# Kernel tuning notes

Hardware: AMD Instinct MI355X
Metric: run time of the kernel (lower is better)

The kernel has to match this reference:

```python
import jax, jax.numpy as jnp
import numpy as np


def setup_inputs() -> dict:
    key = jax.random.key(0)
    k1, k2 = jax.random.split(key)
    x = jax.random.normal(k1, (32, 256, 32, 32), dtype=jnp.float32)
    emb = jax.random.uniform(k2, (256, 2048), dtype=jnp.float32)
    return {"x": x, "emb": emb}


def reference(x, emb):
    # x: (B, D, H, W), emb: (D, K)
    B, D = x.shape[0], x.shape[1]
    spatial = x.shape[2:]
    K = emb.shape[1]
    # flatten latents: (N, D) with N = B*H*W
    xf = jnp.moveaxis(x, 1, -1).reshape(-1, D)
    d2 = (jnp.sum(xf * xf, axis=-1, keepdims=True)
          - 2.0 * (xf @ emb)
          + jnp.sum(emb * emb, axis=0))  # (N, K)
    argmin = jnp.argmin(d2, axis=-1)  # (N,)
    q = jnp.take(emb.T, argmin, axis=0)  # (N, D) nearest codes
    out = q.reshape(B, *spatial, D)
    out = jnp.moveaxis(out, -1, 1)  # (B, D, H, W)
    return out
```

## Files before the change

### kernel.cpp

```cpp
#include <hip/hip_runtime.h>


typedef __attribute__((ext_vector_type(8))) _Float16 half8v;
typedef __attribute__((ext_vector_type(16))) float floatx16;
typedef unsigned int uint;
typedef unsigned short ushort;

#define DD 256
#define KK 2048
#define SS 1024
#define NN 32768
#define MT 128
#define NTT 256
#define CD 32
#define LDA 40
#define MFMA_F16 __builtin_amdgcn_mfma_f32_32x32x16_f16

union HU { _Float16 f; ushort u; };

__device__ __forceinline__ void split16(float v, ushort& h, ushort& l) {
    HU a, b;
    a.f = (_Float16)v;
    b.f = (_Float16)(v - (float)a.f);
    h = a.u; l = b.u;
}

__device__ __forceinline__ uint pk(ushort a, ushort b) {
    return (uint)a | ((uint)b << 16);
}

__global__ __launch_bounds__(256) void hn_kernel(const float* __restrict__ emb,
                                                 float* __restrict__ hn) {
    __shared__ float red[256];
    const int tid = threadIdx.x;
    const int k = blockIdx.x * 32 + (tid & 31);
    const int j = tid >> 5;
    float a = 0.f;
#pragma unroll
    for (int i = 0; i < 32; ++i) {
        float e = emb[(size_t)(j * 32 + i) * KK + k];
        a += e * e;
    }
    red[tid] = a;
    __syncthreads();
    if (j == 0) {
        float s = a;
#pragma unroll
        for (int g = 1; g < 8; ++g) s += red[g * 32 + (tid & 31)];
        hn[k] = 0.5f * s;
    }
}

__global__ __launch_bounds__(256) void pack_emb(const float* __restrict__ emb,
                                                uint4* __restrict__ epk) {
    int idx = blockIdx.x * 256 + threadIdx.x;
    int k = idx & (KK - 1);
    int q = idx >> 11;
    ushort h[8], l[8];
#pragma unroll
    for (int j = 0; j < 8; ++j) {
        float e = emb[(size_t)(8 * q + j) * KK + k];
        split16(e, h[j], l[j]);
    }
    uint4 H, L;
    H.x = pk(h[0], h[1]); H.y = pk(h[2], h[3]);
    H.z = pk(h[4], h[5]); H.w = pk(h[6], h[7]);
    L.x = pk(l[0], l[1]); L.y = pk(l[2], l[3]);
    L.z = pk(l[4], l[5]); L.w = pk(l[6], l[7]);
    epk[(size_t)(q * 2 + 0) * KK + k] = H;
    epk[(size_t)(q * 2 + 1) * KK + k] = L;
}

template <bool PRE>
__global__ __launch_bounds__(1024, 4) void vq_fused(
        const float* __restrict__ x, const float* __restrict__ emb,
        const float* __restrict__ hn, const uint4* __restrict__ epk,
        float* __restrict__ out) {
    __shared__ ushort Ah[2][MT * LDA], Al[2][MT * LDA];
    __shared__ ushort Bh[2][NTT * LDA], Bl[2][NTT * LDA];
    __shared__ float sv[4][MT];
    __shared__ int   sc[4][MT];
    __shared__ int   bc[MT];

    const int tid = threadIdx.x;
    const int lane = tid & 63;
    const int wid = tid >> 6;
    const int colk = lane & 31;
    const int half = lane >> 5;
    const int wm = (wid & 3) * 32;
    const int wn = (wid >> 2) * 64;

    const int base_n = blockIdx.x * MT;
    const int bq = base_n >> 10;
    const int sb = base_n & (SS - 1);

    const int lat_a = tid & 127;
    const int d2a = tid >> 7;
    const int cod_b = tid & 255;
    const int pB = (tid >> 8) & 1;
    const int oB = tid >> 9;

    const float* xA = x + ((size_t)bq * DD + 2 * d2a) * SS + sb + lat_a;

    floatx16 acc[2];
#pragma unroll
    for (int j = 0; j < 2; ++j) acc[j] = (floatx16)(0.0f);

    float bestv[16];
    int bestc[16];
#pragma unroll
    for (int r = 0; r < 16; ++r) { bestv[r] = 3.4e38f; bestc[r] = 0; }

    float fa[4];
    uint4 ub0, ub1;
    float fb[16];

    fa[0] = xA[0];
    fa[1] = xA[SS];
    fa[2] = xA[(size_t)16 * SS];
    fa[3] = xA[(size_t)17 * SS];
    if constexpr (PRE) {
        const int qg = 2 * oB;
        ub0 = epk[(size_t)(qg * 2 + pB) * KK + cod_b];
        ub1 = epk[(size_t)((qg + 1) * 2 + pB) * KK + cod_b];
    } else {
#pragma unroll
        for (int i = 0; i < 16; ++i)
            fb[i] = emb[(size_t)(oB * 16 + i) * KK + cod_b];
    }
    {
        ushort h0, l0, h1, l1, h2, l2, h3, l3;
        split16(fa[0], h0, l0); split16(fa[1], h1, l1);
        split16(fa[2], h2, l2); split16(fa[3], h3, l3);
        *reinterpret_cast<uint*>(&Ah[0][lat_a * LDA + 2 * d2a]) = pk(h0, h1);
        *reinterpret_cast<uint*>(&Al[0][lat_a * LDA + 2 * d2a]) = pk(l0, l1);
        *reinterpret_cast<uint*>(&Ah[0][lat_a * LDA + 2 * d2a + 16]) = pk(h2, h3);
        *reinterpret_cast<uint*>(&Al[0][lat_a * LDA + 2 * d2a + 16]) = pk(l2, l3);
        uint4 w0, w1;
        if constexpr (PRE) {
            w0 = ub0; w1 = ub1;
        } else {
            ushort h[16], l[16];
#pragma unroll
            for (int i = 0; i < 16; ++i) split16(fb[i], h[i], l[i]);
            const ushort* s = pB ? l : h;
            w0.x = pk(s[0], s[1]);  w0.y = pk(s[2], s[3]);
            w0.z = pk(s[4], s[5]);  w0.w = pk(s[6], s[7]);
            w1.x = pk(s[8], s[9]);  w1.y = pk(s[10], s[11]);
            w1.z = pk(s[12], s[13]); w1.w = pk(s[14], s[15]);
        }
        ushort* Bp = pB ? &Bl[0][0] : &Bh[0][0];
        *reinterpret_cast<uint4*>(&Bp[cod_b * LDA + oB * 16]) = w0;
        *reinterpret_cast<uint4*>(&Bp[cod_b * LDA + oB * 16 + 8]) = w1;
    }
    __syncthreads();

    for (int c = 0; c < 64; ++c) {
        const int cur = c & 1, nxt = cur ^ 1;
        if (c < 63) {
            const int c1 = c + 1;
            const int kt1 = c1 >> 3;
            const int dt1 = (c1 & 7) * CD;
            fa[0] = xA[(size_t)(dt1 + 0) * SS];
            fa[1] = xA[(size_t)(dt1 + 1) * SS];
            fa[2] = xA[(size_t)(dt1 + 16) * SS];
            fa[3] = xA[(size_t)(dt1 + 17) * SS];
            if constexpr (PRE) {
                const int qg = (dt1 >> 3) + 2 * oB;
                const size_t kb = (size_t)kt1 * NTT + cod_b;
                ub0 = epk[(size_t)(qg * 2 + pB) * KK + kb];
                ub1 = epk[(size_t)((qg + 1) * 2 + pB) * KK + kb];
            } else {
#pragma unroll
                for (int i = 0; i < 16; ++i)
                    fb[i] = emb[(size_t)(dt1 + oB * 16 + i) * KK
                                + kt1 * NTT + cod_b];
            }
        }
        const int fo = colk * LDA + half * 8;
        {
            half8v ah = *reinterpret_cast<const half8v*>(&Ah[cur][fo + wm * LDA]);
            half8v al = *reinterpret_cast<const half8v*>(&Al[cur][fo + wm * LDA]);
            half8v bh0 = *reinterpret_cast<const half8v*>(&Bh[cur][fo + wn * LDA]);
            half8v bh1 = *reinterpret_cast<const half8v*>(&Bh[cur][fo + (wn + 32) * LDA]);
            half8v bl0 = *reinterpret_cast<const half8v*>(&Bl[cur][fo + wn * LDA]);
            half8v bl1 = *reinterpret_cast<const half8v*>(&Bl[cur][fo + (wn + 32) * LDA]);
            acc[0] = MFMA_F16(ah, bh0, acc[0], 0, 0, 0);
            acc[0] = MFMA_F16(ah, bl0, acc[0], 0, 0, 0);
            acc[0] = MFMA_F16(al, bh0, acc[0], 0, 0, 0);
            acc[1] = MFMA_F16(ah, bh1, acc[1], 0, 0, 0);
            acc[1] = MFMA_F16(ah, bl1, acc[1], 0, 0, 0);
            acc[1] = MFMA_F16(al, bh1, acc[1], 0, 0, 0);
        }
        {
            half8v ah = *reinterpret_cast<const half8v*>(&Ah[cur][fo + wm * LDA + 16]);
            half8v al = *reinterpret_cast<const half8v*>(&Al[cur][fo + wm * LDA + 16]);
            half8v bh0 = *reinterpret_cast<const half8v*>(&Bh[cur][fo + wn * LDA + 16]);
            half8v bh1 = *reinterpret_cast<const half8v*>(&Bh[cur][fo + (wn + 32) * LDA + 16]);
            half8v bl0 = *reinterpret_cast<const half8v*>(&Bl[cur][fo + wn * LDA + 16]);
            half8v bl1 = *reinterpret_cast<const half8v*>(&Bl[cur][fo + (wn + 32) * LDA + 16]);
            acc[0] = MFMA_F16(ah, bh0, acc[0], 0, 0, 0);
            acc[0] = MFMA_F16(ah, bl0, acc[0], 0, 0, 0);
            acc[0] = MFMA_F16(al, bh0, acc[0], 0, 0, 0);
            acc[1] = MFMA_F16(ah, bh1, acc[1], 0, 0, 0);
            acc[1] = MFMA_F16(ah, bl1, acc[1], 0, 0, 0);
            acc[1] = MFMA_F16(al, bh1, acc[1], 0, 0, 0);
        }

        if (c < 63) {
            ushort h0, l0, h1, l1, h2, l2, h3, l3;
            split16(fa[0], h0, l0); split16(fa[1], h1, l1);
            split16(fa[2], h2, l2); split16(fa[3], h3, l3);
            *reinterpret_cast<uint*>(&Ah[nxt][lat_a * LDA + 2 * d2a]) = pk(h0, h1);
            *reinterpret_cast<uint*>(&Al[nxt][lat_a * LDA + 2 * d2a]) = pk(l0, l1);
            *reinterpret_cast<uint*>(&Ah[nxt][lat_a * LDA + 2 * d2a + 16]) = pk(h2, h3);
            *reinterpret_cast<uint*>(&Al[nxt][lat_a * LDA + 2 * d2a + 16]) = pk(l2, l3);
            uint4 w0, w1;
            if constexpr (PRE) {
                w0 = ub0; w1 = ub1;
            } else {
                ushort h[16], l[16];
#pragma unroll
                for (int i = 0; i < 16; ++i) split16(fb[i], h[i], l[i]);
                const ushort* s = pB ? l : h;
                w0.x = pk(s[0], s[1]);  w0.y = pk(s[2], s[3]);
                w0.z = pk(s[4], s[5]);  w0.w = pk(s[6], s[7]);
                w1.x = pk(s[8], s[9]);  w1.y = pk(s[10], s[11]);
                w1.z = pk(s[12], s[13]); w1.w = pk(s[14], s[15]);
            }
            ushort* Bp = pB ? &Bl[nxt][0] : &Bh[nxt][0];
            *reinterpret_cast<uint4*>(&Bp[cod_b * LDA + oB * 16]) = w0;
            *reinterpret_cast<uint4*>(&Bp[cod_b * LDA + oB * 16 + 8]) = w1;
        }
        if ((c & 7) == 7) {
            const int kt = c >> 3;
            const int cd0 = kt * NTT + wn + colk;
            const int cd1 = cd0 + 32;
            const float h0 = hn[cd0];
            const float h1 = hn[cd1];
#pragma unroll
            for (int r = 0; r < 16; ++r) {
                float s0 = h0 - acc[0][r];
                float s1 = h1 - acc[1][r];
                float v = s0; int cd = cd0;
                if (s1 < s0) { v = s1; cd = cd1; }
                if (v < bestv[r]) { bestv[r] = v; bestc[r] = cd; }
                acc[0][r] = 0.f;
                acc[1][r] = 0.f;
            }
        }
        __syncthreads();
    }

#pragma unroll
    for (int r = 0; r < 16; ++r) {
        float v = bestv[r];
        int cd = bestc[r];
#pragma unroll
        for (int mk = 1; mk < 32; mk <<= 1) {
            float ov = __shfl_xor(v, mk);
            int oc = __shfl_xor(cd, mk);
            if (ov < v || (ov == v && oc < cd)) { v = ov; cd = oc; }
        }
        if (colk == 0) {
            const int row = (r & 3) + 8 * (r >> 2) + 4 * half;
            sv[wid >> 2][wm + row] = v;
            sc[wid >> 2][wm + row] = cd;
        }
    }
    __syncthreads();
    if (tid < MT) {
        float v = sv[0][tid]; int cd = sc[0][tid];
#pragma unroll
        for (int g = 1; g < 4; ++g) {
            float ov = sv[g][tid]; int oc = sc[g][tid];
            if (ov < v || (ov == v && oc < cd)) { v = ov; cd = oc; }
        }
        bc[tid] = cd;
    }
    __syncthreads();
    {
        const int mq = tid & 31;
        const int dg = tid >> 5;
        const int k0 = bc[mq * 4 + 0];
        const int k1 = bc[mq * 4 + 1];
        const int k2 = bc[mq * 4 + 2];
        const int k3 = bc[mq * 4 + 3];
#pragma unroll 4
        for (int dd = 0; dd < 8; ++dd) {
            const int d = dg * 8 + dd;
            const float* er = emb + (size_t)d * KK;
            float4 o = make_float4(er[k0], er[k1], er[k2], er[k3]);
            reinterpret_cast<float4*>(&out[((size_t)bq * DD + d) * SS + sb])[mq] = o;
        }
    }
}

extern "C" void kernel_launch(void* const* d_in, const int* in_sizes, int n_in,
                              void* d_out, int out_size, void* d_ws, size_t ws_size,
                              hipStream_t stream) {
    const float* x = (const float*)d_in[0];
    const float* emb = (const float*)d_in[1];
    float* out = (float*)d_out;
    float* hn = (float*)d_ws;
    uint4* epk = (uint4*)((char*)d_ws + KK * sizeof(float));

    const size_t need = (size_t)KK * 4 + (size_t)32 * 2 * KK * 16;

    hipLaunchKernelGGL(hn_kernel, dim3(KK / 32), dim3(256), 0, stream, emb, hn);
    if (ws_size >= need) {
        hipLaunchKernelGGL(pack_emb, dim3(65536 / 256), dim3(256), 0, stream,
                           emb, epk);
        hipLaunchKernelGGL((vq_fused<true>), dim3(NN / MT), dim3(1024), 0, stream,
                           x, emb, hn, epk, out);
    } else {
        hipLaunchKernelGGL((vq_fused<false>), dim3(NN / MT), dim3(1024), 0, stream,
                           x, emb, hn, epk, out);
    }
}
```

Measured before the change: 216.1 us.

## Use 512-thread blocks with 64x64 warp tiles and XOR-swizzled LDS layout

```diff
diff --git a/kernel.cpp b/kernel.cpp
--- a/kernel.cpp
+++ b/kernel.cpp
@@ -13,7 +13,7 @@
 #define MT 128
 #define NTT 256
 #define CD 32
-#define LDA 40
+#define LDB 32
 #define MFMA_F16 __builtin_amdgcn_mfma_f32_32x32x16_f16
 
 union HU { _Float16 f; ushort u; };
@@ -27,6 +27,10 @@
 
 __device__ __forceinline__ uint pk(ushort a, ushort b) {
     return (uint)a | ((uint)b << 16);
+}
+
+__device__ __forceinline__ int swz(int row, int slot) {
+    return row * LDB + ((slot ^ ((row >> 1) & 3)) << 3);
 }
 
 __global__ __launch_bounds__(256) void hn_kernel(const float* __restrict__ emb,
@@ -72,12 +76,12 @@
 }
 
 template <bool PRE>
-__global__ __launch_bounds__(1024, 4) void vq_fused(
+__global__ __launch_bounds__(512, 2) void vq_fused(
         const float* __restrict__ x, const float* __restrict__ emb,
         const float* __restrict__ hn, const uint4* __restrict__ epk,
         float* __restrict__ out) {
-    __shared__ ushort Ah[2][MT * LDA], Al[2][MT * LDA];
-    __shared__ ushort Bh[2][NTT * LDA], Bl[2][NTT * LDA];
+    __shared__ ushort Ah[2][MT * LDB], Al[2][MT * LDB];
+    __shared__ ushort Bh[2][NTT * LDB], Bl[2][NTT * LDB];
     __shared__ float sv[4][MT];
     __shared__ int   sc[4][MT];
     __shared__ int   bc[MT];
@@ -87,71 +91,83 @@
     const int wid = tid >> 6;
     const int colk = lane & 31;
     const int half = lane >> 5;
-    const int wm = (wid & 3) * 32;
-    const int wn = (wid >> 2) * 64;
+    const int wm = (wid & 1) * 64;
+    const int wn = (wid >> 1) * 64;
 
     const int base_n = blockIdx.x * MT;
     const int bq = base_n >> 10;
     const int sb = base_n & (SS - 1);
 
     const int lat_a = tid & 127;
-    const int d2a = tid >> 7;
+    const int qa = tid >> 7;
     const int cod_b = tid & 255;
-    const int pB = (tid >> 8) & 1;
-    const int oB = tid >> 9;
-
-    const float* xA = x + ((size_t)bq * DD + 2 * d2a) * SS + sb + lat_a;
-
-    floatx16 acc[2];
-#pragma unroll
-    for (int j = 0; j < 2; ++j) acc[j] = (floatx16)(0.0f);
-
-    float bestv[16];
-    int bestc[16];
-#pragma unroll
-    for (int r = 0; r < 16; ++r) { bestv[r] = 3.4e38f; bestc[r] = 0; }
-
-    float fa[4];
-    uint4 ub0, ub1;
+    const int pB = tid >> 8;
+    const int oB = tid >> 8;
+
+    const float* xA = x + (size_t)bq * DD * SS + sb + lat_a;
+
+    floatx16 acc[2][2];
+#pragma unroll
+    for (int i = 0; i < 2; ++i)
+#pragma unroll
+        for (int j = 0; j < 2; ++j) acc[i][j] = (floatx16)(0.0f);
+
+    float bestv[2][16];
+    int bestc[2][16];
+#pragma unroll
+    for (int t = 0; t < 2; ++t)
+#pragma unroll
+        for (int r = 0; r < 16; ++r) { bestv[t][r] = 3.4e38f; bestc[t][r] = 0; }
+
+    float fa[8];
+    uint4 uq[4];
     float fb[16];
 
-    fa[0] = xA[0];
-    fa[1] = xA[SS];
-    fa[2] = xA[(size_t)16 * SS];
-    fa[3] = xA[(size_t)17 * SS];
+#pragma unroll
+    for (int j = 0; j < 8; ++j) fa[j] = xA[(size_t)(8 * qa + j) * SS];
     if constexpr (PRE) {
-        const int qg = 2 * oB;
-        ub0 = epk[(size_t)(qg * 2 + pB) * KK + cod_b];
-        ub1 = epk[(size_t)((qg + 1) * 2 + pB) * KK + cod_b];
+#pragma unroll
+        for (int s = 0; s < 4; ++s)
+            uq[s] = epk[(size_t)(s * 2 + pB) * KK + cod_b];
     } else {
 #pragma unroll
         for (int i = 0; i < 16; ++i)
             fb[i] = emb[(size_t)(oB * 16 + i) * KK + cod_b];
     }
     {
-        ushort h0, l0, h1, l1, h2, l2, h3, l3;
-        split16(fa[0], h0, l0); split16(fa[1], h1, l1);
-        split16(fa[2], h2, l2); split16(fa[3], h3, l3);
-        *reinterpret_cast<uint*>(&Ah[0][lat_a * LDA + 2 * d2a]) = pk(h0, h1);
-        *reinterpret_cast<uint*>(&Al[0][lat_a * LDA + 2 * d2a]) = pk(l0, l1);
-        *reinterpret_cast<uint*>(&Ah[0][lat_a * LDA + 2 * d2a + 16]) = pk(h2, h3);
-        *reinterpret_cast<uint*>(&Al[0][lat_a * LDA + 2 * d2a + 16]) = pk(l2, l3);
-        uint4 w0, w1;
+        ushort h[8], l[8];
+#pragma unroll
+        for (int j = 0; j < 8; ++j) split16(fa[j], h[j], l[j]);
+        uint4 H, L;
+        H.x = pk(h[0], h[1]); H.y = pk(h[2], h[3]);
+        H.z = pk(h[4], h[5]); H.w = pk(h[6], h[7]);
+        L.x = pk(l[0], l[1]); L.y = pk(l[2], l[3]);
+        L.z = pk(l[4], l[5]); L.w = pk(l[6], l[7]);
+        *reinterpret_cast<uint4*>(&Ah[0][swz(lat_a, qa)]) = H;
+        *reinterpret_cast<uint4*>(&Al[0][swz(lat_a, qa)]) = L;
         if constexpr (PRE) {
-            w0 = ub0; w1 = ub1;
+            ushort* Bp = pB ? &Bl[0][0] : &Bh[0][0];
+#pragma unroll
+            for (int s = 0; s < 4; ++s)
+                *reinterpret_cast<uint4*>(&Bp[swz(cod_b, s)]) = uq[s];
         } else {
-            ushort h[16], l[16];
-#pragma unroll
-            for (int i = 0; i < 16; ++i) split16(fb[i], h[i], l[i]);
-            const ushort* s = pB ? l : h;
-            w0.x = pk(s[0], s[1]);  w0.y = pk(s[2], s[3]);
-            w0.z = pk(s[4], s[5]);  w0.w = pk(s[6], s[7]);
-            w1.x = pk(s[8], s[9]);  w1.y = pk(s[10], s[11]);
-            w1.z = pk(s[12], s[13]); w1.w = pk(s[14], s[15]);
-        }
-        ushort* Bp = pB ? &Bl[0][0] : &Bh[0][0];
-        *reinterpret_cast<uint4*>(&Bp[cod_b * LDA + oB * 16]) = w0;
-        *reinterpret_cast<uint4*>(&Bp[cod_b * LDA + oB * 16 + 8]) = w1;
+            ushort hh[16], ll[16];
+#pragma unroll
+            for (int i = 0; i < 16; ++i) split16(fb[i], hh[i], ll[i]);
+            uint4 w;
+            w.x = pk(hh[0], hh[1]);  w.y = pk(hh[2], hh[3]);
+            w.z = pk(hh[4], hh[5]);  w.w = pk(hh[6], hh[7]);
+            *reinterpret_cast<uint4*>(&Bh[0][swz(cod_b, oB * 2)]) = w;
+            w.x = pk(hh[8], hh[9]);  w.y = pk(hh[10], hh[11]);
+            w.z = pk(hh[12], hh[13]); w.w = pk(hh[14], hh[15]);
+            *reinterpret_cast<uint4*>(&Bh[0][swz(cod_b, oB * 2 + 1)]) = w;
+            w.x = pk(ll[0], ll[1]);  w.y = pk(ll[2], ll[3]);
+            w.z = pk(ll[4], ll[5]);  w.w = pk(ll[6], ll[7]);
+            *reinterpret_cast<uint4*>(&Bl[0][swz(cod_b, oB * 2)]) = w;
+            w.x = pk(ll[8], ll[9]);  w.y = pk(ll[10], ll[11]);
+            w.z = pk(ll[12], ll[13]); w.w = pk(ll[14], ll[15]);
+            *reinterpret_cast<uint4*>(&Bl[0][swz(cod_b, oB * 2 + 1)]) = w;
+        }
     }
     __syncthreads();
 
@@ -161,15 +177,15 @@
             const int c1 = c + 1;
             const int kt1 = c1 >> 3;
             const int dt1 = (c1 & 7) * CD;
-            fa[0] = xA[(size_t)(dt1 + 0) * SS];
-            fa[1] = xA[(size_t)(dt1 + 1) * SS];
-            fa[2] = xA[(size_t)(dt1 + 16) * SS];
-            fa[3] = xA[(size_t)(dt1 + 17) * SS];
+#pragma unroll
+            for (int j = 0; j < 8; ++j)
+                fa[j] = xA[(size_t)(dt1 + 8 * qa + j) * SS];
             if constexpr (PRE) {
-                const int qg = (dt1 >> 3) + 2 * oB;
+                const int qg = dt1 >> 3;
                 const size_t kb = (size_t)kt1 * NTT + cod_b;
-                ub0 = epk[(size_t)(qg * 2 + pB) * KK + kb];
-                ub1 = epk[(size_t)((qg + 1) * 2 + pB) * KK + kb];
+#pragma unroll
+                for (int s = 0; s < 4; ++s)
+                    uq[s] = epk[(size_t)((qg + s) * 2 + pB) * KK + kb];
             } else {
 #pragma unroll
                 for (int i = 0; i < 16; ++i)
@@ -177,60 +193,69 @@
                                 + kt1 * NTT + cod_b];
             }
         }
-        const int fo = colk * LDA + half * 8;
-        {
-            half8v ah = *reinterpret_cast<const half8v*>(&Ah[cur][fo + wm * LDA]);
-            half8v al = *reinterpret_cast<const half8v*>(&Al[cur][fo + wm * LDA]);
-            half8v bh0 = *reinterpret_cast<const half8v*>(&Bh[cur][fo + wn * LDA]);
-            half8v bh1 = *reinterpret_cast<const half8v*>(&Bh[cur][fo + (wn + 32) * LDA]);
-            half8v bl0 = *reinterpret_cast<const half8v*>(&Bl[cur][fo + wn * LDA]);
-            half8v bl1 = *reinterpret_cast<const half8v*>(&Bl[cur][fo + (wn + 32) * LDA]);
-            acc[0] = MFMA_F16(ah, bh0, acc[0], 0, 0, 0);
-            acc[0] = MFMA_F16(ah, bl0, acc[0], 0, 0, 0);
-            acc[0] = MFMA_F16(al, bh0, acc[0], 0, 0, 0);
-            acc[1] = MFMA_F16(ah, bh1, acc[1], 0, 0, 0);
-            acc[1] = MFMA_F16(ah, bl1, acc[1], 0, 0, 0);
-            acc[1] = MFMA_F16(al, bh1, acc[1], 0, 0, 0);
-        }
-        {
-            half8v ah = *reinterpret_cast<const half8v*>(&Ah[cur][fo + wm * LDA + 16]);
-            half8v al = *reinterpret_cast<const half8v*>(&Al[cur][fo + wm * LDA + 16]);
-            half8v bh0 = *reinterpret_cast<const half8v*>(&Bh[cur][fo + wn * LDA + 16]);
-            half8v bh1 = *reinterpret_cast<const half8v*>(&Bh[cur][fo + (wn + 32) * LDA + 16]);
-            half8v bl0 = *reinterpret_cast<const half8v*>(&Bl[cur][fo + wn * LDA + 16]);
-            half8v bl1 = *reinterpret_cast<const half8v*>(&Bl[cur][fo + (wn + 32) * LDA + 16]);
-            acc[0] = MFMA_F16(ah, bh0, acc[0], 0, 0, 0);
-            acc[0] = MFMA_F16(ah, bl0, acc[0], 0, 0, 0);
-            acc[0] = MFMA_F16(al, bh0, acc[0], 0, 0, 0);
-            acc[1] = MFMA_F16(ah, bh1, acc[1], 0, 0, 0);
-            acc[1] = MFMA_F16(ah, bl1, acc[1], 0, 0, 0);
-            acc[1] = MFMA_F16(al, bh1, acc[1], 0, 0, 0);
+#pragma unroll
+        for (int t = 0; t < 2; ++t) {
+            const int sA = t * 2 + half;
+            half8v ah0 = *reinterpret_cast<const half8v*>(&Ah[cur][swz(wm + colk, sA)]);
+            half8v ah1 = *reinterpret_cast<const half8v*>(&Ah[cur][swz(wm + 32 + colk, sA)]);
+            half8v al0 = *reinterpret_cast<const half8v*>(&Al[cur][swz(wm + colk, sA)]);
+            half8v al1 = *reinterpret_cast<const half8v*>(&Al[cur][swz(wm + 32 + colk, sA)]);
+            half8v bh0 = *reinterpret_cast<const half8v*>(&Bh[cur][swz(wn + colk, sA)]);
+            half8v bh1 = *reinterpret_cast<const half8v*>(&Bh[cur][swz(wn + 32 + colk, sA)]);
+            half8v bl0 = *reinterpret_cast<const half8v*>(&Bl[cur][swz(wn + colk, sA)]);
+            half8v bl1 = *reinterpret_cast<const half8v*>(&Bl[cur][swz(wn + 32 + colk, sA)]);
+
+            acc[0][0] = MFMA_F16(ah0, bh0, acc[0][0], 0, 0, 0);
+            acc[0][0] = MFMA_F16(ah0, bl0, acc[0][0], 0, 0, 0);
+            acc[0][0] = MFMA_F16(al0, bh0, acc[0][0], 0, 0, 0);
+
+            acc[0][1] = MFMA_F16(ah0, bh1, acc[0][1], 0, 0, 0);
+            acc[0][1] = MFMA_F16(ah0, bl1, acc[0][1], 0, 0, 0);
+            acc[0][1] = MFMA_F16(al0, bh1, acc[0][1], 0, 0, 0);
+
+            acc[1][0] = MFMA_F16(ah1, bh0, acc[1][0], 0, 0, 0);
+            acc[1][0] = MFMA_F16(ah1, bl0, acc[1][0], 0, 0, 0);
+            acc[1][0] = MFMA_F16(al1, bh0, acc[1][0], 0, 0, 0);
+
+            acc[1][1] = MFMA_F16(ah1, bh1, acc[1][1], 0, 0, 0);
+            acc[1][1] = MFMA_F16(ah1, bl1, acc[1][1], 0, 0, 0);
+            acc[1][1] = MFMA_F16(al1, bh1, acc[1][1], 0, 0, 0);
         }
 
         if (c < 63) {
-            ushort h0, l0, h1, l1, h2, l2, h3, l3;
-            split16(fa[0], h0, l0); split16(fa[1], h1, l1);
-            split16(fa[2], h2, l2); split16(fa[3], h3, l3);
-            *reinterpret_cast<uint*>(&Ah[nxt][lat_a * LDA + 2 * d2a]) = pk(h0, h1);
-            *reinterpret_cast<uint*>(&Al[nxt][lat_a * LDA + 2 * d2a]) = pk(l0, l1);
-            *reinterpret_cast<uint*>(&Ah[nxt][lat_a * LDA + 2 * d2a + 16]) = pk(h2, h3);
-            *reinterpret_cast<uint*>(&Al[nxt][lat_a * LDA + 2 * d2a + 16]) = pk(l2, l3);
-            uint4 w0, w1;
+            ushort h[8], l[8];
+#pragma unroll
+            for (int j = 0; j < 8; ++j) split16(fa[j], h[j], l[j]);
+            uint4 H, L;
+            H.x = pk(h[0], h[1]); H.y = pk(h[2], h[3]);
+            H.z = pk(h[4], h[5]); H.w = pk(h[6], h[7]);
+            L.x = pk(l[0], l[1]); L.y = pk(l[2], l[3]);
+            L.z = pk(l[4], l[5]); L.w = pk(l[6], l[7]);
+            *reinterpret_cast<uint4*>(&Ah[nxt][swz(lat_a, qa)]) = H;
+            *reinterpret_cast<uint4*>(&Al[nxt][swz(lat_a, qa)]) = L;
             if constexpr (PRE) {
-                w0 = ub0; w1 = ub1;
+                ushort* Bp = pB ? &Bl[nxt][0] : &Bh[nxt][0];
+#pragma unroll
+                for (int s = 0; s < 4; ++s)
+                    *reinterpret_cast<uint4*>(&Bp[swz(cod_b, s)]) = uq[s];
             } else {
-                ushort h[16], l[16];
-#pragma unroll
-                for (int i = 0; i < 16; ++i) split16(fb[i], h[i], l[i]);
-                const ushort* s = pB ? l : h;
-                w0.x = pk(s[0], s[1]);  w0.y = pk(s[2], s[3]);
-                w0.z = pk(s[4], s[5]);  w0.w = pk(s[6], s[7]);
-                w1.x = pk(s[8], s[9]);  w1.y = pk(s[10], s[11]);
-                w1.z = pk(s[12], s[13]); w1.w = pk(s[14], s[15]);
-            }
-            ushort* Bp = pB ? &Bl[nxt][0] : &Bh[nxt][0];
-            *reinterpret_cast<uint4*>(&Bp[cod_b * LDA + oB * 16]) = w0;
-            *reinterpret_cast<uint4*>(&Bp[cod_b * LDA + oB * 16 + 8]) = w1;
+                ushort hh[16], ll[16];
+#pragma unroll
+                for (int i = 0; i < 16; ++i) split16(fb[i], hh[i], ll[i]);
+                uint4 w;
+                w.x = pk(hh[0], hh[1]);  w.y = pk(hh[2], hh[3]);
+                w.z = pk(hh[4], hh[5]);  w.w = pk(hh[6], hh[7]);
+                *reinterpret_cast<uint4*>(&Bh[nxt][swz(cod_b, oB * 2)]) = w;
+                w.x = pk(hh[8], hh[9]);  w.y = pk(hh[10], hh[11]);
+                w.z = pk(hh[12], hh[13]); w.w = pk(hh[14], hh[15]);
+                *reinterpret_cast<uint4*>(&Bh[nxt][swz(cod_b, oB * 2 + 1)]) = w;
+                w.x = pk(ll[0], ll[1]);  w.y = pk(ll[2], ll[3]);
+                w.z = pk(ll[4], ll[5]);  w.w = pk(ll[6], ll[7]);
+                *reinterpret_cast<uint4*>(&Bl[nxt][swz(cod_b, oB * 2)]) = w;
+                w.x = pk(ll[8], ll[9]);  w.y = pk(ll[10], ll[11]);
+                w.z = pk(ll[12], ll[13]); w.w = pk(ll[14], ll[15]);
+                *reinterpret_cast<uint4*>(&Bl[nxt][swz(cod_b, oB * 2 + 1)]) = w;
+            }
         }
         if ((c & 7) == 7) {
             const int kt = c >> 3;
@@ -239,33 +264,39 @@
             const float h0 = hn[cd0];
             const float h1 = hn[cd1];
 #pragma unroll
-            for (int r = 0; r < 16; ++r) {
-                float s0 = h0 - acc[0][r];
-                float s1 = h1 - acc[1][r];
-                float v = s0; int cd = cd0;
-                if (s1 < s0) { v = s1; cd = cd1; }
-                if (v < bestv[r]) { bestv[r] = v; bestc[r] = cd; }
-                acc[0][r] = 0.f;
-                acc[1][r] = 0.f;
+            for (int tm = 0; tm < 2; ++tm) {
+#pragma unroll
+                for (int r = 0; r < 16; ++r) {
+                    float s0 = h0 - acc[tm][0][r];
+                    float s1 = h1 - acc[tm][1][r];
+                    float v = s0; int cd = cd0;
+                    if (s1 < s0) { v = s1; cd = cd1; }
+                    if (v < bestv[tm][r]) { bestv[tm][r] = v; bestc[tm][r] = cd; }
+                    acc[tm][0][r] = 0.f;
+                    acc[tm][1][r] = 0.f;
+                }
             }
         }
         __syncthreads();
     }
 
 #pragma unroll
-    for (int r = 0; r < 16; ++r) {
-        float v = bestv[r];
-        int cd = bestc[r];
-#pragma unroll
-        for (int mk = 1; mk < 32; mk <<= 1) {
-            float ov = __shfl_xor(v, mk);
-            int oc = __shfl_xor(cd, mk);
-            if (ov < v || (ov == v && oc < cd)) { v = ov; cd = oc; }
-        }
-        if (colk == 0) {
-            const int row = (r & 3) + 8 * (r >> 2) + 4 * half;
-            sv[wid >> 2][wm + row] = v;
-            sc[wid >> 2][wm + row] = cd;
+    for (int tm = 0; tm < 2; ++tm) {
+#pragma unroll
+        for (int r = 0; r < 16; ++r) {
+            float v = bestv[tm][r];
+            int cd = bestc[tm][r];
+#pragma unroll
+            for (int mk = 1; mk < 32; mk <<= 1) {
+                float ov = __shfl_xor(v, mk);
+                int oc = __shfl_xor(cd, mk);
+                if (ov < v || (ov == v && oc < cd)) { v = ov; cd = oc; }
+            }
+            if (colk == 0) {
+                const int row = (r & 3) + 8 * (r >> 2) + 4 * half;
+                sv[wid >> 1][wm + tm * 32 + row] = v;
+                sc[wid >> 1][wm + tm * 32 + row] = cd;
+            }
         }
     }
     __syncthreads();
@@ -287,8 +318,8 @@
         const int k2 = bc[mq * 4 + 2];
         const int k3 = bc[mq * 4 + 3];
 #pragma unroll 4
-        for (int dd = 0; dd < 8; ++dd) {
-            const int d = dg * 8 + dd;
+        for (int dd = 0; dd < 16; ++dd) {
+            const int d = dg * 16 + dd;
             const float* er = emb + (size_t)d * KK;
             float4 o = make_float4(er[k0], er[k1], er[k2], er[k3]);
             reinterpret_cast<float4*>(&out[((size_t)bq * DD + d) * SS + sb])[mq] = o;
@@ -311,10 +342,10 @@
     if (ws_size >= need) {
         hipLaunchKernelGGL(pack_emb, dim3(65536 / 256), dim3(256), 0, stream,
                            emb, epk);
-        hipLaunchKernelGGL((vq_fused<true>), dim3(NN / MT), dim3(1024), 0, stream,
+        hipLaunchKernelGGL((vq_fused<true>), dim3(NN / MT), dim3(512), 0, stream,
                            x, emb, hn, epk, out);
     } else {
-        hipLaunchKernelGGL((vq_fused<false>), dim3(NN / MT), dim3(1024), 0, stream,
+        hipLaunchKernelGGL((vq_fused<false>), dim3(NN / MT), dim3(512), 0, stream,
                            x, emb, hn, epk, out);
     }
 }
```

After: 220.3 us. About the same (+2.0%).

## Prefetch global tiles two stages ahead with register double-buffering

Applied to the files above, without the earlier changes.

```diff
diff --git a/kernel.cpp b/kernel.cpp
--- a/kernel.cpp
+++ b/kernel.cpp
@@ -111,144 +111,113 @@
 #pragma unroll
     for (int r = 0; r < 16; ++r) { bestv[r] = 3.4e38f; bestc[r] = 0; }
 
-    float fa[4];
-    uint4 ub0, ub1;
-    float fb[16];
-
-    fa[0] = xA[0];
-    fa[1] = xA[SS];
-    fa[2] = xA[(size_t)16 * SS];
-    fa[3] = xA[(size_t)17 * SS];
-    if constexpr (PRE) {
-        const int qg = 2 * oB;
-        ub0 = epk[(size_t)(qg * 2 + pB) * KK + cod_b];
-        ub1 = epk[(size_t)((qg + 1) * 2 + pB) * KK + cod_b];
-    } else {
-#pragma unroll
-        for (int i = 0; i < 16; ++i)
-            fb[i] = emb[(size_t)(oB * 16 + i) * KK + cod_b];
-    }
-    {
+    float fa0[4], fa1[4];
+    uint4 u00, u01, u10, u11;
+    float fb0[16], fb1[16];
+
+    auto issueA = [&](int c, float (&fa)[4]) {
+        const int dt = (c & 7) * CD;
+        fa[0] = xA[(size_t)(dt + 0) * SS];
+        fa[1] = xA[(size_t)(dt + 1) * SS];
+        fa[2] = xA[(size_t)(dt + 16) * SS];
+        fa[3] = xA[(size_t)(dt + 17) * SS];
+    };
+    auto issueB = [&](int c, uint4& a0, uint4& a1, float (&fb)[16]) {
+        const int kt = c >> 3;
+        const int dt = (c & 7) * CD;
+        if constexpr (PRE) {
+            const int qg = (dt >> 3) + 2 * oB;
+            const size_t kb = (size_t)kt * NTT + cod_b;
+            a0 = epk[(size_t)(qg * 2 + pB) * KK + kb];
+            a1 = epk[(size_t)((qg + 1) * 2 + pB) * KK + kb];
+        } else {
+#pragma unroll
+            for (int i = 0; i < 16; ++i)
+                fb[i] = emb[(size_t)(dt + oB * 16 + i) * KK
+                            + (size_t)kt * NTT + cod_b];
+        }
+    };
+    auto stageWrite = [&](int nxt, float (&fa)[4], uint4& a0, uint4& a1,
+                          float (&fb)[16]) {
         ushort h0, l0, h1, l1, h2, l2, h3, l3;
         split16(fa[0], h0, l0); split16(fa[1], h1, l1);
         split16(fa[2], h2, l2); split16(fa[3], h3, l3);
-        *reinterpret_cast<uint*>(&Ah[0][lat_a * LDA + 2 * d2a]) = pk(h0, h1);
-        *reinterpret_cast<uint*>(&Al[0][lat_a * LDA + 2 * d2a]) = pk(l0, l1);
-        *reinterpret_cast<uint*>(&Ah[0][lat_a * LDA + 2 * d2a + 16]) = pk(h2, h3);
-        *reinterpret_cast<uint*>(&Al[0][lat_a * LDA + 2 * d2a + 16]) = pk(l2, l3);
+        *reinterpret_cast<uint*>(&Ah[nxt][lat_a * LDA + 2 * d2a]) = pk(h0, h1);
+        *reinterpret_cast<uint*>(&Al[nxt][lat_a * LDA + 2 * d2a]) = pk(l0, l1);
+        *reinterpret_cast<uint*>(&Ah[nxt][lat_a * LDA + 2 * d2a + 16]) = pk(h2, h3);
+        *reinterpret_cast<uint*>(&Al[nxt][lat_a * LDA + 2 * d2a + 16]) = pk(l2, l3);
         uint4 w0, w1;
         if constexpr (PRE) {
-            w0 = ub0; w1 = ub1;
+            w0 = a0; w1 = a1;
         } else {
-            ushort h[16], l[16];
-#pragma unroll
-            for (int i = 0; i < 16; ++i) split16(fb[i], h[i], l[i]);
-            const ushort* s = pB ? l : h;
-            w0.x = pk(s[0], s[1]);  w0.y = pk(s[2], s[3]);
-            w0.z = pk(s[4], s[5]);  w0.w = pk(s[6], s[7]);
-            w1.x = pk(s[8], s[9]);  w1.y = pk(s[10], s[11]);
+            ushort hh[16], ll[16];
+#pragma unroll
+            for (int i = 0; i < 16; ++i) split16(fb[i], hh[i], ll[i]);
+            const ushort* s = pB ? ll : hh;
+            w0.x = pk(s[0], s[1]);   w0.y = pk(s[2], s[3]);
+            w0.z = pk(s[4], s[5]);   w0.w = pk(s[6], s[7]);
+            w1.x = pk(s[8], s[9]);   w1.y = pk(s[10], s[11]);
             w1.z = pk(s[12], s[13]); w1.w = pk(s[14], s[15]);
         }
-        ushort* Bp = pB ? &Bl[0][0] : &Bh[0][0];
+        ushort* Bp = pB ? &Bl[nxt][0] : &Bh[nxt][0];
         *reinterpret_cast<uint4*>(&Bp[cod_b * LDA + oB * 16]) = w0;
         *reinterpret_cast<uint4*>(&Bp[cod_b * LDA + oB * 16 + 8]) = w1;
-    }
-    __syncthreads();
-
-    for (int c = 0; c < 64; ++c) {
-        const int cur = c & 1, nxt = cur ^ 1;
-        if (c < 63) {
-            const int c1 = c + 1;
-            const int kt1 = c1 >> 3;
-            const int dt1 = (c1 & 7) * CD;
-            fa[0] = xA[(size_t)(dt1 + 0) * SS];
-            fa[1] = xA[(size_t)(dt1 + 1) * SS];
-            fa[2] = xA[(size_t)(dt1 + 16) * SS];
-            fa[3] = xA[(size_t)(dt1 + 17) * SS];
-            if constexpr (PRE) {
-                const int qg = (dt1 >> 3) + 2 * oB;
-                const size_t kb = (size_t)kt1 * NTT + cod_b;
-                ub0 = epk[(size_t)(qg * 2 + pB) * KK + kb];
-                ub1 = epk[(size_t)((qg + 1) * 2 + pB) * KK + kb];
-            } else {
-#pragma unroll
-                for (int i = 0; i < 16; ++i)
-                    fb[i] = emb[(size_t)(dt1 + oB * 16 + i) * KK
-                                + kt1 * NTT + cod_b];
-            }
-        }
+    };
+    auto compute = [&](int cur) {
         const int fo = colk * LDA + half * 8;
-        {
-            half8v ah = *reinterpret_cast<const half8v*>(&Ah[cur][fo + wm * LDA]);
-            half8v al = *reinterpret_cast<const half8v*>(&Al[cur][fo + wm * LDA]);
-            half8v bh0 = *reinterpret_cast<const half8v*>(&Bh[cur][fo + wn * LDA]);
-            half8v bh1 = *reinterpret_cast<const half8v*>(&Bh[cur][fo + (wn + 32) * LDA]);
-            half8v bl0 = *reinterpret_cast<const half8v*>(&Bl[cur][fo + wn * LDA]);
-            half8v bl1 = *reinterpret_cast<const half8v*>(&Bl[cur][fo + (wn + 32) * LDA]);
+#pragma unroll
+        for (int t = 0; t < 2; ++t) {
+            const int o = t * 16;
+            half8v ah = *reinterpret_cast<const half8v*>(&Ah[cur][fo + wm * LDA + o]);
+            half8v al = *reinterpret_cast<const half8v*>(&Al[cur][fo + wm * LDA + o]);
+            half8v bh0 = *reinterpret_cast<const half8v*>(&Bh[cur][fo + wn * LDA + o]);
+            half8v bh1 = *reinterpret_cast<const half8v*>(&Bh[cur][fo + (wn + 32) * LDA + o]);
+            half8v bl0 = *reinterpret_cast<const half8v*>(&Bl[cur][fo + wn * LDA + o]);
+            half8v bl1 = *reinterpret_cast<const half8v*>(&Bl[cur][fo + (wn + 32) * LDA + o]);
+
             acc[0] = MFMA_F16(ah, bh0, acc[0], 0, 0, 0);
             acc[0] = MFMA_F16(ah, bl0, acc[0], 0, 0, 0);
             acc[0] = MFMA_F16(al, bh0, acc[0], 0, 0, 0);
+
             acc[1] = MFMA_F16(ah, bh1, acc[1], 0, 0, 0);
             acc[1] = MFMA_F16(ah, bl1, acc[1], 0, 0, 0);
             acc[1] = MFMA_F16(al, bh1, acc[1], 0, 0, 0);
         }
-        {
-            half8v ah = *reinterpret_cast<const half8v*>(&Ah[cur][fo + wm * LDA + 16]);
-            half8v al = *reinterpret_cast<const half8v*>(&Al[cur][fo + wm * LDA + 16]);
-            half8v bh0 = *reinterpret_cast<const half8v*>(&Bh[cur][fo + wn * LDA + 16]);
-            half8v bh1 = *reinterpret_cast<const half8v*>(&Bh[cur][fo + (wn + 32) * LDA + 16]);
-            half8v bl0 = *reinterpret_cast<const half8v*>(&Bl[cur][fo + wn * LDA + 16]);
-            half8v bl1 = *reinterpret_cast<const half8v*>(&Bl[cur][fo + (wn + 32) * LDA + 16]);
-            acc[0] = MFMA_F16(ah, bh0, acc[0], 0, 0, 0);
-            acc[0] = MFMA_F16(ah, bl0, acc[0], 0, 0, 0);
-            acc[0] = MFMA_F16(al, bh0, acc[0], 0, 0, 0);
-            acc[1] = MFMA_F16(ah, bh1, acc[1], 0, 0, 0);
-            acc[1] = MFMA_F16(ah, bl1, acc[1], 0, 0, 0);
-            acc[1] = MFMA_F16(al, bh1, acc[1], 0, 0, 0);
-        }
-
-        if (c < 63) {
-            ushort h0, l0, h1, l1, h2, l2, h3, l3;
-            split16(fa[0], h0, l0); split16(fa[1], h1, l1);
-            split16(fa[2], h2, l2); split16(fa[3], h3, l3);
-            *reinterpret_cast<uint*>(&Ah[nxt][lat_a * LDA + 2 * d2a]) = pk(h0, h1);
-            *reinterpret_cast<uint*>(&Al[nxt][lat_a * LDA + 2 * d2a]) = pk(l0, l1);
-            *reinterpret_cast<uint*>(&Ah[nxt][lat_a * LDA + 2 * d2a + 16]) = pk(h2, h3);
-            *reinterpret_cast<uint*>(&Al[nxt][lat_a * LDA + 2 * d2a + 16]) = pk(l2, l3);
-            uint4 w0, w1;
-            if constexpr (PRE) {
-                w0 = ub0; w1 = ub1;
-            } else {
-                ushort h[16], l[16];
-#pragma unroll
-                for (int i = 0; i < 16; ++i) split16(fb[i], h[i], l[i]);
-                const ushort* s = pB ? l : h;
-                w0.x = pk(s[0], s[1]);  w0.y = pk(s[2], s[3]);
-                w0.z = pk(s[4], s[5]);  w0.w = pk(s[6], s[7]);
-                w1.x = pk(s[8], s[9]);  w1.y = pk(s[10], s[11]);
-                w1.z = pk(s[12], s[13]); w1.w = pk(s[14], s[15]);
-            }
-            ushort* Bp = pB ? &Bl[nxt][0] : &Bh[nxt][0];
-            *reinterpret_cast<uint4*>(&Bp[cod_b * LDA + oB * 16]) = w0;
-            *reinterpret_cast<uint4*>(&Bp[cod_b * LDA + oB * 16 + 8]) = w1;
-        }
-        if ((c & 7) == 7) {
-            const int kt = c >> 3;
-            const int cd0 = kt * NTT + wn + colk;
-            const int cd1 = cd0 + 32;
-            const float h0 = hn[cd0];
-            const float h1 = hn[cd1];
-#pragma unroll
-            for (int r = 0; r < 16; ++r) {
-                float s0 = h0 - acc[0][r];
-                float s1 = h1 - acc[1][r];
-                float v = s0; int cd = cd0;
-                if (s1 < s0) { v = s1; cd = cd1; }
-                if (v < bestv[r]) { bestv[r] = v; bestc[r] = cd; }
-                acc[0][r] = 0.f;
-                acc[1][r] = 0.f;
-            }
-        }
+    };
+    auto epilogue = [&](int kt) {
+        const int cd0 = kt * NTT + wn + colk;
+        const int cd1 = cd0 + 32;
+        const float h0 = hn[cd0];
+        const float h1 = hn[cd1];
+#pragma unroll
+        for (int r = 0; r < 16; ++r) {
+            float s0 = h0 - acc[0][r];
+            float s1 = h1 - acc[1][r];
+            float v = s0; int cd = cd0;
+            if (s1 < s0) { v = s1; cd = cd1; }
+            if (v < bestv[r]) { bestv[r] = v; bestc[r] = cd; }
+            acc[0][r] = 0.f;
+            acc[1][r] = 0.f;
+        }
+    };
+
+    issueA(0, fa0); issueB(0, u00, u01, fb0);
+    stageWrite(0, fa0, u00, u01, fb0);
+    issueA(1, fa1); issueB(1, u10, u11, fb1);
+    __syncthreads();
+
+    for (int cc = 0; cc < 32; ++cc) {
+        const int c0 = cc * 2;
+        if (c0 + 2 < 64) { issueA(c0 + 2, fa0); issueB(c0 + 2, u00, u01, fb0); }
+        stageWrite(1, fa1, u10, u11, fb1);
+        compute(0);
+        __syncthreads();
+
+        const int c1 = c0 + 1;
+        if (c1 + 2 < 64) { issueA(c1 + 2, fa1); issueB(c1 + 2, u10, u11, fb1); }
+        if (c1 + 1 < 64) { stageWrite(0, fa0, u00, u01, fb0); }
+        compute(1);
+        if ((c1 & 7) == 7) epilogue(c1 >> 3);
         __syncthreads();
     }
 
```

Result: faster. 211.5 us (-2.1%).
